# Kernel optimization log

Hardware: AMD Instinct MI355X
Metric: run time of the kernel (lower is better)

Reference implementation:

```python
import jax, jax.numpy as jnp
import numpy as np

N, F, H, E = 10000, 256, 256, 320000
TEMPERATURE = 1.0


def setup_inputs() -> dict:
    key = jax.random.key(0)
    k_x, k_ei, k_w1, k_b1, k_w2, k_b2 = jax.random.split(key, 6)
    x = jax.random.normal(k_x, (N, F), dtype=jnp.float32)
    edge_index = jax.random.randint(k_ei, (2, E), 0, N, dtype=jnp.int64)
    # PyTorch nn.Linear default init: U(-1/sqrt(fan_in), 1/sqrt(fan_in)), weight shape (out, in)
    lim1 = 1.0 / np.sqrt(2 * F)
    W1 = jax.random.uniform(k_w1, (H, 2 * F), dtype=jnp.float32, minval=-lim1, maxval=lim1)
    b1 = jax.random.uniform(k_b1, (H,), dtype=jnp.float32, minval=-lim1, maxval=lim1)
    lim2 = 1.0 / np.sqrt(H)
    W2 = jax.random.uniform(k_w2, (1, H), dtype=jnp.float32, minval=-lim2, maxval=lim2)
    b2 = jax.random.uniform(k_b2, (1,), dtype=jnp.float32, minval=-lim2, maxval=lim2)
    return {"x": x, "edge_index": edge_index, "W1": W1, "b1": b1, "W2": W2, "b2": b2}


def reference(x, edge_index, W1, b1, W2, b2):
    row, col = edge_index[0], edge_index[1]
    edge_feat = jnp.concatenate([x[row], x[col]], axis=-1)  # (E, 2F)
    h = jax.nn.relu(edge_feat @ W1.T + b1)                  # (E, H)
    logits = (h @ W2.T + b2).squeeze(-1)                    # (E,)
    m = jax.nn.sigmoid(logits / max(TEMPERATURE, 1e-6))
    return m
```

## Files before the change

kernel.cpp:

```cpp
#include <hip/hip_runtime.h>
#include <hip/hip_bf16.h>


typedef __attribute__((ext_vector_type(8))) short bf16x8;
typedef __attribute__((ext_vector_type(4))) float f32x4;

__device__ __forceinline__ unsigned short f2bf(float f) {
    __hip_bfloat16 h = __float2bfloat16(f);
    return *reinterpret_cast<unsigned short*>(&h);
}

__global__ __launch_bounds__(256) void convert_w(const float* __restrict__ w1,
                                                 unsigned short* __restrict__ wb,
                                                 int nw4) {
    int i = blockIdx.x * 256 + threadIdx.x;
    if (i < nw4) {
        float4 v = ((const float4*)w1)[i];
        ushort4 o = {f2bf(v.x), f2bf(v.y), f2bf(v.z), f2bf(v.w)};
        ((ushort4*)wb)[i] = o;
    }
}

__global__ __launch_bounds__(256) void gemm_mfma(const float* __restrict__ x,
                                                 const unsigned short* __restrict__ wb,
                                                 const float* __restrict__ b1,
                                                 unsigned short* __restrict__ uv,
                                                 int M) {
    __shared__ __align__(16) unsigned short As[2][16][40];

    const int t    = threadIdx.x;
    const int wave = t >> 6;
    const int lane = t & 63;
    const int lm   = lane & 15;
    const int lq   = lane >> 4;
    const int lk   = lq * 8;
    const int m0   = blockIdx.x * 16;

    const int srow = t >> 4;
    const int sk   = (t & 15) * 2;
    const int grow = m0 + srow;
    const float* sptr = x + (size_t)(grow < M ? grow : (M - 1)) * 256 + sk;

    const int half    = wave >> 1;
    const int colbase = wave * 128;
    const int rowbase = (wave & 1) * 128;
    const unsigned short* bpre =
        wb + (size_t)(rowbase + lm) * 512 + half * 256 + lk;

    f32x4 acc[8];
#pragma unroll
    for (int j = 0; j < 8; ++j) acc[j] = f32x4{0.f, 0.f, 0.f, 0.f};

    float2 apref = *(const float2*)(sptr);

#pragma unroll
    for (int it = 0; it < 8; ++it) {
        const int kt  = it * 32;
        const int cur = it & 1;
        unsigned int lo = ((unsigned int)f2bf(apref.x));
        unsigned int hi = ((unsigned int)f2bf(apref.y)) << 16;
        *(unsigned int*)&As[cur][srow][sk] = lo | hi;
        if (it < 7) apref = *(const float2*)(sptr + kt + 32);
        __syncthreads();
        bf16x8 a = *(const bf16x8*)&As[cur][lm][lk];
#pragma unroll
        for (int j = 0; j < 8; ++j) {
            bf16x8 b = *(const bf16x8*)(bpre + (size_t)j * 16 * 512 + kt);
            acc[j] = __builtin_amdgcn_mfma_f32_16x16x32_bf16(a, b, acc[j], 0, 0, 0);
        }
    }

    const int row0 = m0 + lq * 4;
#pragma unroll
    for (int j = 0; j < 8; ++j) {
        const int col  = colbase + j * 16 + lm;
        const float badd = half ? 0.f : b1[col];
#pragma unroll
        for (int r = 0; r < 4; ++r) {
            if (row0 + r < M)
                uv[(size_t)(row0 + r) * 512 + col] = f2bf(acc[j][r] + badd);
        }
    }
}

__global__ __launch_bounds__(256) void edge_kernel(const unsigned short* __restrict__ uv,
                                                   const int* __restrict__ ei,
                                                   const float* __restrict__ w2,
                                                   const float* __restrict__ b2p,
                                                   float* __restrict__ out, int E) {
    const int lane = threadIdx.x & 63;
    const int g = lane >> 4;
    const int c = lane & 15;
    const int wid  = (blockIdx.x * blockDim.x + threadIdx.x) >> 6;
    const int nwav = (gridDim.x * blockDim.x) >> 6;
    const int nb   = E >> 2;

    float w2r[16];
#pragma unroll
    for (int i = 0; i < 4; ++i)
        *(float4*)&w2r[i * 4] = *(const float4*)(w2 + c * 16 + i * 4);
    const float b2 = b2p[0];

    for (int b = wid; b < nb; b += 2 * nwav) {
        const int bB = b + nwav;
        const bool has2 = bB < nb;

        const int e0 = b * 4 + g;
        const int r0 = ei[e0];
        const int c0 = ei[E + e0];
        const int e1 = has2 ? bB * 4 + g : e0;
        const int r1 = ei[e1];
        const int c1 = ei[E + e1];

        const uint4* up0 = (const uint4*)(uv + (size_t)r0 * 512 + c * 16);
        const uint4* vp0 = (const uint4*)(uv + (size_t)c0 * 512 + 256 + c * 16);
        const uint4* up1 = (const uint4*)(uv + (size_t)r1 * 512 + c * 16);
        const uint4* vp1 = (const uint4*)(uv + (size_t)c1 * 512 + 256 + c * 16);

        uint4 ua0 = up0[0], ua1 = up0[1];
        uint4 va0 = vp0[0], va1 = vp0[1];
        uint4 ub0 = up1[0], ub1 = up1[1];
        uint4 vb0 = vp1[0], vb1 = vp1[1];

        unsigned int uw[8], vw[8];
        float2 p2;
        float p;

        *(uint4*)&uw[0] = ua0; *(uint4*)&uw[4] = ua1;
        *(uint4*)&vw[0] = va0; *(uint4*)&vw[4] = va1;
        p2 = float2{0.f, 0.f};
#pragma unroll
        for (int i = 0; i < 8; ++i) {
            float2 u2 = {__uint_as_float(uw[i] << 16),
                         __uint_as_float(uw[i] & 0xffff0000u)};
            float2 v2 = {__uint_as_float(vw[i] << 16),
                         __uint_as_float(vw[i] & 0xffff0000u)};
            float2 s2 = {fmaxf(u2.x + v2.x, 0.f), fmaxf(u2.y + v2.y, 0.f)};
            p2.x = fmaf(s2.x, w2r[2 * i], p2.x);
            p2.y = fmaf(s2.y, w2r[2 * i + 1], p2.y);
        }
        p = p2.x + p2.y;
#pragma unroll
        for (int off = 1; off < 16; off <<= 1)
            p += __shfl_xor(p, off, 64);
        if (c == 0) out[e0] = 1.f / (1.f + __expf(-(p + b2)));

        if (has2) {
            *(uint4*)&uw[0] = ub0; *(uint4*)&uw[4] = ub1;
            *(uint4*)&vw[0] = vb0; *(uint4*)&vw[4] = vb1;
            p2 = float2{0.f, 0.f};
#pragma unroll
            for (int i = 0; i < 8; ++i) {
                float2 u2 = {__uint_as_float(uw[i] << 16),
                             __uint_as_float(uw[i] & 0xffff0000u)};
                float2 v2 = {__uint_as_float(vw[i] << 16),
                             __uint_as_float(vw[i] & 0xffff0000u)};
                float2 s2 = {fmaxf(u2.x + v2.x, 0.f), fmaxf(u2.y + v2.y, 0.f)};
                p2.x = fmaf(s2.x, w2r[2 * i], p2.x);
                p2.y = fmaf(s2.y, w2r[2 * i + 1], p2.y);
            }
            p = p2.x + p2.y;
#pragma unroll
            for (int off = 1; off < 16; off <<= 1)
                p += __shfl_xor(p, off, 64);
            if (c == 0) out[e1] = 1.f / (1.f + __expf(-(p + b2)));
        }
    }
}

extern "C" void kernel_launch(void* const* d_in, const int* in_sizes, int n_in,
                              void* d_out, int out_size, void* d_ws, size_t ws_size,
                              hipStream_t stream) {
    const float* x  = (const float*)d_in[0];
    const int*   ei = (const int*)d_in[1];
    const float* W1 = (const float*)d_in[2];
    const float* b1 = (const float*)d_in[3];
    const float* W2 = (const float*)d_in[4];
    const float* b2 = (const float*)d_in[5];
    float* out = (float*)d_out;

    const int N = in_sizes[0] / 256;
    const int E = in_sizes[1] / 2;

    unsigned short* uv = (unsigned short*)d_ws;
    unsigned short* wb = uv + (size_t)N * 512;

    const int nw4 = (256 * 512) / 4;
    convert_w<<<(nw4 + 255) / 256, 256, 0, stream>>>(W1, wb, nw4);

    gemm_mfma<<<(N + 15) / 16, 256, 0, stream>>>(x, wb, b1, uv, N);

    edge_kernel<<<2048, 256, 0, stream>>>(uv, ei, W2, b2, out, E);
}
```

Before: 131.0 us.

## Bucket-sort edges by source row before the edge gather kernel

```diff
diff --git a/kernel.cpp b/kernel.cpp
--- a/kernel.cpp
+++ b/kernel.cpp
@@ -8,6 +8,45 @@
 __device__ __forceinline__ unsigned short f2bf(float f) {
     __hip_bfloat16 h = __float2bfloat16(f);
     return *reinterpret_cast<unsigned short*>(&h);
+}
+
+#define NBUCK 625
+
+__global__ __launch_bounds__(256) void hist_kernel(const int* __restrict__ ei,
+                                                   int* __restrict__ counts, int E) {
+    int e = blockIdx.x * 256 + threadIdx.x;
+    if (e < E) atomicAdd(&counts[ei[e] >> 4], 1);
+}
+
+__global__ __launch_bounds__(1024) void scan_kernel(const int* __restrict__ counts,
+                                                    int* __restrict__ cursor) {
+    __shared__ int s[1024];
+    int t = threadIdx.x;
+    s[t] = (t < NBUCK) ? counts[t] : 0;
+    __syncthreads();
+#pragma unroll
+    for (int d = 1; d < 1024; d <<= 1) {
+        int v = (t >= d) ? s[t - d] : 0;
+        __syncthreads();
+        s[t] += v;
+        __syncthreads();
+    }
+    if (t < NBUCK) cursor[t] = (t == 0) ? 0 : s[t - 1];
+}
+
+__global__ __launch_bounds__(256) void scatter_kernel(const int* __restrict__ ei,
+                                                      int* __restrict__ cursor,
+                                                      int* __restrict__ srow,
+                                                      int* __restrict__ scol,
+                                                      int* __restrict__ sidx, int E) {
+    int e = blockIdx.x * 256 + threadIdx.x;
+    if (e < E) {
+        int row = ei[e];
+        int pos = atomicAdd(&cursor[row >> 4], 1);
+        srow[pos] = row;
+        scol[pos] = ei[E + e];
+        sidx[pos] = e;
+    }
 }
 
 __global__ __launch_bounds__(256) void convert_w(const float* __restrict__ w1,
@@ -84,7 +123,9 @@
 }
 
 __global__ __launch_bounds__(256) void edge_kernel(const unsigned short* __restrict__ uv,
-                                                   const int* __restrict__ ei,
+                                                   const int* __restrict__ srowp,
+                                                   const int* __restrict__ scolp,
+                                                   const int* __restrict__ sidxp,
                                                    const float* __restrict__ w2,
                                                    const float* __restrict__ b2p,
                                                    float* __restrict__ out, int E) {
@@ -105,12 +146,14 @@
         const int bB = b + nwav;
         const bool has2 = bB < nb;
 
-        const int e0 = b * 4 + g;
-        const int r0 = ei[e0];
-        const int c0 = ei[E + e0];
-        const int e1 = has2 ? bB * 4 + g : e0;
-        const int r1 = ei[e1];
-        const int c1 = ei[E + e1];
+        const int p0 = b * 4 + g;
+        const int r0 = srowp[p0];
+        const int c0 = scolp[p0];
+        const int i0 = sidxp[p0];
+        const int p1 = has2 ? bB * 4 + g : p0;
+        const int r1 = srowp[p1];
+        const int c1 = scolp[p1];
+        const int i1 = sidxp[p1];
 
         const uint4* up0 = (const uint4*)(uv + (size_t)r0 * 512 + c * 16);
         const uint4* vp0 = (const uint4*)(uv + (size_t)c0 * 512 + 256 + c * 16);
@@ -143,7 +186,7 @@
 #pragma unroll
         for (int off = 1; off < 16; off <<= 1)
             p += __shfl_xor(p, off, 64);
-        if (c == 0) out[e0] = 1.f / (1.f + __expf(-(p + b2)));
+        if (c == 0) out[i0] = 1.f / (1.f + __expf(-(p + b2)));
 
         if (has2) {
             *(uint4*)&uw[0] = ub0; *(uint4*)&uw[4] = ub1;
@@ -163,7 +206,7 @@
 #pragma unroll
             for (int off = 1; off < 16; off <<= 1)
                 p += __shfl_xor(p, off, 64);
-            if (c == 0) out[e1] = 1.f / (1.f + __expf(-(p + b2)));
+            if (c == 0) out[i1] = 1.f / (1.f + __expf(-(p + b2)));
         }
     }
 }
@@ -184,11 +227,21 @@
 
     unsigned short* uv = (unsigned short*)d_ws;
     unsigned short* wb = uv + (size_t)N * 512;
+    int* counts = (int*)(wb + 256 * 512);
+    int* cursor = counts + NBUCK;
+    int* srow   = cursor + NBUCK;
+    int* scol   = srow + E;
+    int* sidx   = scol + E;
+
+    hipMemsetAsync(counts, 0, NBUCK * sizeof(int), stream);
+    hist_kernel<<<(E + 255) / 256, 256, 0, stream>>>(ei, counts, E);
+    scan_kernel<<<1, 1024, 0, stream>>>(counts, cursor);
+    scatter_kernel<<<(E + 255) / 256, 256, 0, stream>>>(ei, cursor, srow, scol, sidx, E);
 
     const int nw4 = (256 * 512) / 4;
     convert_w<<<(nw4 + 255) / 256, 256, 0, stream>>>(W1, wb, nw4);
 
     gemm_mfma<<<(N + 15) / 16, 256, 0, stream>>>(x, wb, b1, uv, N);
 
-    edge_kernel<<<2048, 256, 0, stream>>>(uv, ei, W2, b2, out, E);
-}
+    edge_kernel<<<2048, 256, 0, stream>>>(uv, srow, scol, sidx, W2, b2, out, E);
+}
```

Result: slower. 315.1 us (+140.5%).
